# Performance work log

Measured on AMD Instinct MI355X. Metric: run time of the kernel, lower is better.

Reference implementation:

```python
import jax, jax.numpy as jnp
import numpy as np

B, V, C, H, W, D, G = 1, 5, 32, 128, 160, 48, 1


def _bilinear_sample(fea, x, y):
    # fea: [B,C,H,W]; x,y: [B,N] pixel coords (grid_sample align_corners=True, zero padding)
    Bb, Cc, Hh, Ww = fea.shape
    x0 = jnp.floor(x); y0 = jnp.floor(y)
    x1 = x0 + 1.0; y1 = y0 + 1.0
    wx1 = x - x0; wx0 = 1.0 - wx1
    wy1 = y - y0; wy0 = 1.0 - wy1
    flat = fea.reshape(Bb, Cc, Hh * Ww)
    def gather(xi, yi):
        valid = (xi >= 0) & (xi <= Ww - 1) & (yi >= 0) & (yi <= Hh - 1)
        xc = jnp.clip(xi, 0, Ww - 1).astype(jnp.int32)
        yc = jnp.clip(yi, 0, Hh - 1).astype(jnp.int32)
        idx = (yc * Ww + xc)[:, None, :]                      # [B,1,N]
        g = jnp.take_along_axis(flat, idx, axis=2)            # [B,C,N]
        return g * valid[:, None, :].astype(fea.dtype)
    return (gather(x0, y0) * (wx0 * wy0)[:, None, :]
          + gather(x1, y0) * (wx1 * wy0)[:, None, :]
          + gather(x0, y1) * (wx0 * wy1)[:, None, :]
          + gather(x1, y1) * (wx1 * wy1)[:, None, :])          # [B,C,N]


def _homo_warp(src_fea, src_proj, ref_proj, depth_values):
    # src_fea [B,C,H,W]; src_proj/ref_proj [B,4,4]; depth_values [B,D,H,W]
    Bb, Cc, Hh, Ww = src_fea.shape
    Dd = depth_values.shape[1]
    proj = src_proj @ jnp.linalg.inv(ref_proj)
    rot, trans = proj[:, :3, :3], proj[:, :3, 3:4]
    yy, xx = jnp.meshgrid(jnp.arange(Hh, dtype=src_fea.dtype),
                          jnp.arange(Ww, dtype=src_fea.dtype), indexing='ij')
    xyz = jnp.stack([xx.ravel(), yy.ravel(), jnp.ones(Hh * Ww, src_fea.dtype)], 0)  # [3,HW]
    rot_xyz = jnp.einsum('bij,jn->bin', rot, xyz)                                    # [B,3,HW]
    d = depth_values.reshape(Bb, 1, Dd, Hh * Ww)
    pxyz = rot_xyz[:, :, None, :] * d + trans[:, :, :, None]                         # [B,3,D,HW]
    px = (pxyz[:, 0] / pxyz[:, 2]).reshape(Bb, -1)
    py = (pxyz[:, 1] / pxyz[:, 2]).reshape(Bb, -1)
    warped = _bilinear_sample(src_fea, px, py)                                       # [B,C,D*HW]
    return warped.reshape(Bb, Cc, Dd, Hh, Ww)


def _pixelwise_net(sim, w0, b0, w1, b1, w2, b2):
    # sim [B,G,D,H,W]; 1x1x1 convs; BatchNorm at default init in eval is identity
    x = jax.nn.relu(jnp.einsum('oc,bcdhw->bodhw', w0, sim) + b0[None, :, None, None, None])
    x = jax.nn.relu(jnp.einsum('oc,bcdhw->bodhw', w1, x) + b1[None, :, None, None, None])
    x = jnp.einsum('oc,bcdhw->bodhw', w2, x) + b2[None, :, None, None, None]
    p = jax.nn.sigmoid(x[:, 0])                       # [B,D,H,W]
    return jnp.max(p, axis=1, keepdims=True)          # [B,1,H,W]


def _fuse_proj(p):
    # p [B,2,4,4] -> extrinsics with K folded into top 3x4
    top = jnp.einsum('bij,bjk->bik', p[:, 1, :3, :3], p[:, 0, :3, :4])
    return p[:, 0].at[:, :3, :4].set(top)


def _forward(features, proj_matrices, depth_values, w0, b0, w1, b1, w2, b2, reg_w, reg_b, num_depth):
    ref_fea = features[0]
    Bb, Cc, Hh, Ww = ref_fea.shape
    ref_proj = _fuse_proj(proj_matrices[:, 0])
    ref_vol = ref_fea.reshape(Bb, G, Cc // G, 1, Hh, Ww)
    sim_sum = 0.0
    wsum = 1e-5
    vw_list = []
    for i in range(1, features.shape[0]):
        src_proj = _fuse_proj(proj_matrices[:, i])
        warped = _homo_warp(features[i], src_proj, ref_proj, depth_values)
        warped = warped.reshape(Bb, G, Cc // G, num_depth, Hh, Ww)
        sim = (warped * ref_vol).mean(2)              # [B,G,D,H,W]
        vw = _pixelwise_net(sim, w0, b0, w1, b1, w2, b2)   # [B,1,H,W]
        vw_list.append(vw)
        sim_sum = sim_sum + sim * vw[:, None]
        wsum = wsum + vw[:, None]
    sim = sim_sum / wsum
    cost = jax.lax.conv_general_dilated(sim, reg_w, (1, 1, 1), 'SAME',
                                        dimension_numbers=('NCDHW', 'OIDHW', 'NCDHW'))
    prob_volume_pre = cost[:, 0] + reg_b[0]           # [B,D,H,W]
    prob = jax.nn.softmax(prob_volume_pre, axis=1)
    idx = jnp.argmax(prob, axis=1, keepdims=True)
    depth = jnp.take_along_axis(depth_values, idx, axis=1)[:, 0]   # winner-take-all depth
    conf = jnp.max(prob, axis=1)
    view_weights = jnp.concatenate(vw_list, axis=1)
    return depth, conf, prob, view_weights


def setup_inputs() -> dict:
    key = jax.random.key(0)
    ks = jax.random.split(key, 6)
    features = jax.random.normal(ks[0], (V, B, C, H, W), jnp.float32)
    # Plausible camera geometry: identity-ish extrinsics + pinhole intrinsics
    K = np.eye(4, dtype=np.float32)
    K[0, 0] = K[1, 1] = 150.0; K[0, 2] = W / 2.0; K[1, 2] = H / 2.0
    mats = []
    for v in range(V):
        E = np.eye(4, dtype=np.float32)
        a = 0.01 * v
        ca, sa = np.cos(a), np.sin(a)
        E[:3, :3] = np.array([[ca, 0, sa], [0, 1, 0], [-sa, 0, ca]], np.float32)
        E[0, 3] = -5.0 * v
        mats.append(np.stack([E, K], 0))
    proj_matrices = jnp.asarray(np.stack(mats, 0)[None])  # [1,V,2,4,4]
    depth_values = jnp.broadcast_to(
        jnp.linspace(425.0, 935.0, D, dtype=jnp.float32).reshape(1, D, 1, 1), (B, D, H, W)) * jnp.ones((B, D, H, W), jnp.float32)
    return {
        'features': features,
        'proj_matrices': proj_matrices,
        'depth_values': depth_values,
        'w0': jax.random.normal(ks[1], (16, G), jnp.float32) * 0.1,
        'b0': jnp.zeros((16,), jnp.float32),
        'w1': jax.random.normal(ks[2], (8, 16), jnp.float32) * 0.1,
        'b1': jnp.zeros((8,), jnp.float32),
        'w2': jax.random.normal(ks[3], (1, 8), jnp.float32) * 0.1,
        'b2': jnp.zeros((1,), jnp.float32),
        'reg_w': jax.random.normal(ks[4], (1, G, 3, 3, 3), jnp.float32) * 0.1,
        'reg_b': jnp.zeros((1,), jnp.float32),
        'num_depth': D,
    }


def reference(features, proj_matrices, depth_values, w0, b0, w1, b1, w2, b2, reg_w, reg_b, num_depth):
    return _forward(features, proj_matrices, depth_values, w0, b0, w1, b1, w2, b2, reg_w, reg_b, num_depth)
```

## Files before the change

kernel.cpp:

```cpp
#include <hip/hip_runtime.h>
#include <hip/hip_bf16.h>
#include <math.h>

#define W_  160
#define H_  128
#define HW  20480
#define D_  48
#define C_  32
#define NV  4

#define TX  16
#define TY  4
#define TXH 18
#define TYH 6
#define NCOL (TXH*TYH)

template<int CTRL>
__device__ __forceinline__ float dpp_add(float s) {
  int t = __builtin_amdgcn_update_dpp(0, __float_as_int(s), CTRL, 0xF, 0xF, true);
  return s + __int_as_float(t);
}

__device__ __forceinline__ unsigned ordf(float f) {
  unsigned b = __float_as_uint(f);
  return b ^ (((int)b >> 31) | 0x80000000u);
}
__device__ __forceinline__ float deordf(unsigned u) {
  unsigned b = (u & 0x80000000u) ? (u ^ 0x80000000u) : ~u;
  return __uint_as_float(b);
}

__device__ __forceinline__ void fuse_proj(const float* pm, float* P) {
  const float* E = pm;
  const float* K = pm + 16;
  for (int r = 0; r < 3; ++r)
    for (int c = 0; c < 4; ++c)
      P[r*4+c] = K[r*4+0]*E[0*4+c] + K[r*4+1]*E[1*4+c] + K[r*4+2]*E[2*4+c];
  for (int c = 0; c < 4; ++c) P[12+c] = E[12+c];
}

__device__ void invert4(const float* m, float* invOut) {
  float inv[16];
  inv[0]  =  m[5]*m[10]*m[15] - m[5]*m[11]*m[14] - m[9]*m[6]*m[15] + m[9]*m[7]*m[14] + m[13]*m[6]*m[11] - m[13]*m[7]*m[10];
  inv[4]  = -m[4]*m[10]*m[15] + m[4]*m[11]*m[14] + m[8]*m[6]*m[15] - m[8]*m[7]*m[14] - m[12]*m[6]*m[11] + m[12]*m[7]*m[10];
  inv[8]  =  m[4]*m[9]*m[15]  - m[4]*m[11]*m[13] - m[8]*m[5]*m[15] + m[8]*m[7]*m[13] + m[12]*m[5]*m[11] - m[12]*m[7]*m[9];
  inv[12] = -m[4]*m[9]*m[14]  + m[4]*m[10]*m[13] + m[8]*m[5]*m[14] - m[8]*m[6]*m[13] - m[12]*m[5]*m[10] + m[12]*m[6]*m[9];
  inv[1]  = -m[1]*m[10]*m[15] + m[1]*m[11]*m[14] + m[9]*m[2]*m[15] - m[9]*m[3]*m[14] - m[13]*m[2]*m[11] + m[13]*m[3]*m[10];
  inv[5]  =  m[0]*m[10]*m[15] - m[0]*m[11]*m[14] - m[8]*m[2]*m[15] + m[8]*m[3]*m[14] + m[12]*m[2]*m[11] - m[12]*m[3]*m[10];
  inv[9]  = -m[0]*m[9]*m[15]  + m[0]*m[11]*m[13] + m[8]*m[1]*m[15] - m[8]*m[3]*m[13] - m[12]*m[1]*m[11] + m[12]*m[3]*m[9];
  inv[13] =  m[0]*m[9]*m[14]  - m[0]*m[10]*m[13] - m[8]*m[1]*m[14] + m[8]*m[2]*m[13] + m[12]*m[1]*m[10] - m[12]*m[2]*m[9];
  inv[2]  =  m[1]*m[6]*m[15]  - m[1]*m[7]*m[14]  - m[5]*m[2]*m[15] + m[5]*m[3]*m[14] + m[13]*m[2]*m[7]  - m[13]*m[3]*m[6];
  inv[6]  = -m[0]*m[6]*m[15]  + m[0]*m[7]*m[14]  + m[4]*m[2]*m[15] - m[4]*m[3]*m[14] - m[12]*m[2]*m[7]  + m[12]*m[3]*m[6];
  inv[10] =  m[0]*m[5]*m[15]  - m[0]*m[7]*m[13]  - m[4]*m[1]*m[15] + m[4]*m[3]*m[13] + m[12]*m[1]*m[7]  - m[12]*m[3]*m[5];
  inv[14] = -m[0]*m[5]*m[14]  + m[0]*m[6]*m[13]  + m[4]*m[1]*m[14] - m[4]*m[2]*m[13] - m[12]*m[1]*m[6]  + m[12]*m[2]*m[5];
  inv[3]  = -m[1]*m[6]*m[11]  + m[1]*m[7]*m[10]  + m[5]*m[2]*m[11] - m[5]*m[3]*m[10] - m[9]*m[2]*m[7]   + m[9]*m[3]*m[6];
  inv[7]  =  m[0]*m[6]*m[11]  - m[0]*m[7]*m[10]  - m[4]*m[2]*m[11] + m[4]*m[3]*m[10] + m[8]*m[2]*m[7]   - m[8]*m[3]*m[6];
  inv[11] = -m[0]*m[5]*m[11]  + m[0]*m[7]*m[9]   + m[4]*m[1]*m[11] - m[4]*m[3]*m[9]  - m[8]*m[1]*m[7]   + m[8]*m[3]*m[5];
  inv[15] =  m[0]*m[5]*m[10]  - m[0]*m[6]*m[9]   - m[4]*m[1]*m[10] + m[4]*m[2]*m[9]  + m[8]*m[1]*m[6]   - m[8]*m[2]*m[5];
  float det = m[0]*inv[0] + m[1]*inv[4] + m[2]*inv[8] + m[3]*inv[12];
  det = 1.0f / det;
  for (int i = 0; i < 16; i++) invOut[i] = inv[i] * det;
}

__global__ void __launch_bounds__(256)
k_prep(const float* __restrict__ feat, const float* __restrict__ pm,
       float* __restrict__ tf, float* __restrict__ xf,
       unsigned* __restrict__ vwu) {
  __shared__ float tile[C_][64+1];
  int v  = blockIdx.y;
  int p0 = blockIdx.x * 64;
  int t  = threadIdx.x;

  if (v == 0) vwu[blockIdx.x*256 + t] = 0u;

  int pl = t & 63;
  int cg = t >> 6;
  const float* src = feat + (size_t)v*C_*HW + p0 + pl;
  #pragma unroll
  for (int k = 0; k < 8; ++k) {
    int c = cg*8 + k;
    tile[c][pl] = src[(size_t)c*HW];
  }
  __syncthreads();

  int pp = t >> 2;
  int co = (t & 3) * 8;
  float4 a, b;
  a.x = tile[co+0][pp]; a.y = tile[co+1][pp]; a.z = tile[co+2][pp]; a.w = tile[co+3][pp];
  b.x = tile[co+4][pp]; b.y = tile[co+5][pp]; b.z = tile[co+6][pp]; b.w = tile[co+7][pp];
  float* dst = tf + ((size_t)v*HW + p0 + pp)*C_ + co;
  *(float4*)dst = a;
  *(float4*)(dst+4) = b;

  if (blockIdx.x == 0 && v == 0) {
    if (t < 64) tf[(size_t)5*HW*C_ + t] = 0.0f;
    if (t == 0) {
      float Pr[16], Pinv[16], Ps[16], M[16];
      fuse_proj(pm, Pr);
      invert4(Pr, Pinv);
      for (int vv = 1; vv <= NV; ++vv) {
        fuse_proj(pm + vv*32, Ps);
        for (int r = 0; r < 4; ++r)
          for (int c = 0; c < 4; ++c) {
            float acc = 0.f;
            for (int k = 0; k < 4; ++k) acc += Ps[r*4+k]*Pinv[k*4+c];
            M[r*4+c] = acc;
          }
        float* o = xf + (vv-1)*12;
        o[0]=M[0];  o[1]=M[1];  o[2]=M[2];
        o[3]=M[4];  o[4]=M[5];  o[5]=M[6];
        o[6]=M[8];  o[7]=M[9];  o[8]=M[10];
        o[9]=M[3];  o[10]=M[7]; o[11]=M[11];
      }
    }
  }
}

template<int KX>
__device__ __forceinline__ void build_tab(
    const char* tfb, int chb, int ZB, float4 rfc,
    int xmin, int ymin, int ch, float* tabp ) {
  #pragma unroll
  for (int t = 0; t < KX*3; ++t) {
    int xi = xmin + t/3;
    int yi = ymin + t%3;
    bool valid = ((unsigned)xi < (unsigned)W_) && ((unsigned)yi < (unsigned)H_);
    int off = valid ? (yi*W_ + xi)*(C_*4) : ZB;
    float4 a = *(const float4*)(tfb + off + chb);
    float d = a.x*rfc.x + a.y*rfc.y + a.z*rfc.z + a.w*rfc.w;
    d = dpp_add<0xB1>(d);
    d = dpp_add<0x4E>(d);
    d = dpp_add<0x141>(d);
    if (ch == (t & 7)) tabp[t] = d;
  }
}

__global__ void __launch_bounds__(256)
k_warp(const float* __restrict__ tf, const float* __restrict__ dv,
       const float* __restrict__ xf, float* __restrict__ sim_all) {
  __shared__ float dtab[4][8][25];

  int lane = threadIdx.x & 63;
  int wv = threadIdx.x >> 6;
  int ch = lane & 7;
  int pix = (lane >> 3) & 7;
  int wvg = __builtin_amdgcn_readfirstlane((blockIdx.x*256 + threadIdx.x) >> 6);
  const int PGPV = HW/8;
  int pg = wvg % PGPV;
  int v  = wvg / PGPV;
  int p  = pg*8 + pix;

  float xpix = (float)(p % W_);
  float ypix = (float)(p / W_);

  const float* M = xf + v*12;
  float rx = M[0]*xpix + M[1]*ypix + M[2];
  float ry = M[3]*xpix + M[4]*ypix + M[5];
  float rz = M[6]*xpix + M[7]*ypix + M[8];
  float t0 = M[9], t1 = M[10], t2 = M[11];

  float4 rfc = *(const float4*)(tf + (size_t)p*C_ + ch*4);
  rfc.x *= (1.0f/(float)C_); rfc.y *= (1.0f/(float)C_);
  rfc.z *= (1.0f/(float)C_); rfc.w *= (1.0f/(float)C_);

  const char* tfb = (const char*)(tf + (size_t)(v+1)*HW*C_);
  const int chb = ch*16;
  const int ZB = (4-v)*HW*C_*4;

  float depE0 = dv[p];
  float depE1 = dv[(size_t)47*HW + p];
  float dpk[6];
  #pragma unroll
  for (int k = 0; k < 6; ++k) dpk[k] = dv[(size_t)(k*8 + ch)*HW + p];

  float Z0 = rz*depE0 + t2, Z1 = rz*depE1 + t2;
  float iz0 = 1.0f / Z0,     iz1 = 1.0f / Z1;
  float pxa = (rx*depE0 + t0) * iz0, pya = (ry*depE0 + t1) * iz0;
  float pxb = (rx*depE1 + t0) * iz1, pyb = (ry*depE1 + t1) * iz1;
  int xmin = (int)floorf(fminf(pxa, pxb));
  int ymin = (int)floorf(fminf(pya, pyb));
  int Nx = (int)floorf(fmaxf(pxa, pxb)) - xmin + 2;
  int Ny = (int)floorf(fmaxf(pya, pyb)) - ymin + 2;

  float dmn = fminf(depE0, depE1), dmx = fmaxf(depE0, depE1);
  bool ok = (Nx <= 8) && (Ny <= 3) && (Z0*Z1 > 0.0f);
  #pragma unroll
  for (int k = 0; k < 6; ++k) ok = ok && (dpk[k] >= dmn) && (dpk[k] <= dmx);

  float* simv = sim_all + (size_t)v*D_*HW + p;

  if (__all(ok)) {
    float* tabp = dtab[wv][pix];
    if (__all(Nx <= 5)) build_tab<5>(tfb, chb, ZB, rfc, xmin, ymin, ch, tabp);
    else                build_tab<8>(tfb, chb, ZB, rfc, xmin, ymin, ch, tabp);

    int xhi = xmin + 6;
    if (__all(Nx <= 5)) xhi = xmin + 3;

    #pragma unroll
    for (int k = 0; k < 6; ++k) {
      float dep = dpk[k];
      float Z  = rz*dep + t2;
      float zr = 1.0f / Z;
      float px = (rx*dep + t0) * zr;
      float py = (ry*dep + t1) * zr;
      int xi = (int)floorf(px);
      int yi = (int)floorf(py);
      xi = min(max(xi, xmin), xhi);
      yi = min(max(yi, ymin), ymin + 1);
      float wx1 = px - (float)xi;
      float wy1 = py - (float)yi;
      float wx0 = 1.0f - wx1, wy0 = 1.0f - wy1;
      int idx = (xi - xmin)*3 + (yi - ymin);
      float t00 = tabp[idx];
      float t01 = tabp[idx + 3];
      float t10 = tabp[idx + 1];
      float t11 = tabp[idx + 4];
      float s = wx0*wy0*t00 + wx1*wy0*t01 + wx0*wy1*t10 + wx1*wy1*t11;
      simv[(size_t)(k*8 + ch)*HW] = s;
    }
  } else {
    const float* tff  = tf + (size_t)(v+1)*HW*C_;
    const float* refp = tf + (size_t)p*C_;
    const int ZE = (4-v)*HW*C_;
    #pragma unroll 1
    for (int k = 0; k < 6; ++k) {
      float dep = dpk[k];
      float Z  = rz*dep + t2;
      float px = (rx*dep + t0) / Z;
      float py = (ry*dep + t1) / Z;
      float x0f = floorf(px), y0f = floorf(py);
      float wx1 = px - x0f, wy1 = py - y0f;
      float wx0 = 1.0f - wx1, wy0 = 1.0f - wy1;
      int x0 = (int)x0f, y0 = (int)y0f;
      int x1 = x0 + 1,   y1 = y0 + 1;
      bool vx0 = ((unsigned)x0 <= (unsigned)(W_-1));
      bool vx1 = ((unsigned)x1 <= (unsigned)(W_-1));
      bool vy0 = ((unsigned)y0 <= (unsigned)(H_-1));
      bool vy1 = ((unsigned)y1 <= (unsigned)(H_-1));
      int cx0 = min(max(x0, 0), W_-1);
      int cx1 = min(max(x1, 0), W_-1);
      int cy0 = min(max(y0, 0), H_-1);
      int cy1 = min(max(y1, 0), H_-1);
      int o00 = (vx0 && vy0) ? (cy0*W_+cx0)*C_ : ZE;
      int o01 = (vx1 && vy0) ? (cy0*W_+cx1)*C_ : ZE;
      int o10 = (vx0 && vy1) ? (cy1*W_+cx0)*C_ : ZE;
      int o11 = (vx1 && vy1) ? (cy1*W_+cx1)*C_ : ZE;
      float a00=0.f, a01=0.f, a10=0.f, a11=0.f;
      #pragma unroll 1
      for (int q = 0; q < 8; ++q) {
        float4 rq = *(const float4*)(refp + q*4);
        float4 c0 = *(const float4*)(tff + o00 + q*4);
        float4 c1 = *(const float4*)(tff + o01 + q*4);
        float4 c2 = *(const float4*)(tff + o10 + q*4);
        float4 c3 = *(const float4*)(tff + o11 + q*4);
        a00 += c0.x*rq.x + c0.y*rq.y + c0.z*rq.z + c0.w*rq.w;
        a01 += c1.x*rq.x + c1.y*rq.y + c1.z*rq.z + c1.w*rq.w;
        a10 += c2.x*rq.x + c2.y*rq.y + c2.z*rq.z + c2.w*rq.w;
        a11 += c3.x*rq.x + c3.y*rq.y + c3.z*rq.z + c3.w*rq.w;
      }
      float s = (wx0*wy0*a00 + wx1*wy0*a01 + wx0*wy1*a10 + wx1*wy1*a11)
                * (1.0f/(float)C_);
      simv[(size_t)(k*8 + ch)*HW] = s;
    }
  }
}

__global__ void __launch_bounds__(256)
k_mlp(const float* __restrict__ sim_all,
      const float* __restrict__ w0, const float* __restrict__ b0,
      const float* __restrict__ w1, const float* __restrict__ b1,
      const float* __restrict__ w2, const float* __restrict__ b2,
      unsigned* __restrict__ vwu) {
  int idx = blockIdx.x*blockDim.x + threadIdx.x;
  if (idx >= NV*(D_/4)*HW) return;
  int p = idx % HW;
  int t = idx / HW;
  int v = t / (D_/4);
  int c = t % (D_/4);

  const float* sp_ = sim_all + ((size_t)(v*D_ + c*4))*HW + p;
  float sv[4];
  sv[0] = sp_[0];
  sv[1] = sp_[HW];
  sv[2] = sp_[2*HW];
  sv[3] = sp_[3*HW];

  float ymax = -3.0e38f;
  #pragma unroll
  for (int k = 0; k < 4; ++k) {
    float s = sv[k];
    float acc0 = b1[0], acc1 = b1[1], acc2 = b1[2], acc3 = b1[3];
    float acc4 = b1[4], acc5 = b1[5], acc6 = b1[6], acc7 = b1[7];
    #pragma unroll
    for (int o = 0; o < 16; ++o) {
      float h = fmaxf(fmaf(w0[o], s, b0[o]), 0.0f);
      acc0 = fmaf(w1[0*16+o], h, acc0);
      acc1 = fmaf(w1[1*16+o], h, acc1);
      acc2 = fmaf(w1[2*16+o], h, acc2);
      acc3 = fmaf(w1[3*16+o], h, acc3);
      acc4 = fmaf(w1[4*16+o], h, acc4);
      acc5 = fmaf(w1[5*16+o], h, acc5);
      acc6 = fmaf(w1[6*16+o], h, acc6);
      acc7 = fmaf(w1[7*16+o], h, acc7);
    }
    float yv = b2[0];
    yv = fmaf(w2[0], fmaxf(acc0, 0.0f), yv);
    yv = fmaf(w2[1], fmaxf(acc1, 0.0f), yv);
    yv = fmaf(w2[2], fmaxf(acc2, 0.0f), yv);
    yv = fmaf(w2[3], fmaxf(acc3, 0.0f), yv);
    yv = fmaf(w2[4], fmaxf(acc4, 0.0f), yv);
    yv = fmaf(w2[5], fmaxf(acc5, 0.0f), yv);
    yv = fmaf(w2[6], fmaxf(acc6, 0.0f), yv);
    yv = fmaf(w2[7], fmaxf(acc7, 0.0f), yv);
    ymax = fmaxf(ymax, yv);
  }
  atomicMax(&vwu[(size_t)v*HW + p], ordf(ymax));
}

__global__ void __launch_bounds__(256)
k_fct(const float* __restrict__ sim_all, const unsigned* __restrict__ vwu,
      const float* __restrict__ rw, const float* __restrict__ rb,
      const float* __restrict__ dv, float* __restrict__ out) {
  __shared__ float sfus[D_][TYH][TXH+1];
  __shared__ float scost[D_][64];
  __shared__ float svw[NV][NCOL];
  __shared__ float sinvw[NCOL];
  __shared__ int   sgpc[NCOL];

  int tid = threadIdx.x;
  int gx0 = blockIdx.x*TX;
  int gy0 = blockIdx.y*TY;

  if (tid < NCOL) {
    int yy = tid / TXH, xx = tid % TXH;
    int gy = gy0 + yy - 1, gx = gx0 + xx - 1;
    bool valid = (gx >= 0) && (gx < W_) && (gy >= 0) && (gy < H_);
    int gp = min(max(gy,0),H_-1)*W_ + min(max(gx,0),W_-1);
    sgpc[tid] = gp;
    float a0 = 1.0f/(1.0f + expf(-deordf(vwu[0*HW+gp])));
    float a1 = 1.0f/(1.0f + expf(-deordf(vwu[1*HW+gp])));
    float a2 = 1.0f/(1.0f + expf(-deordf(vwu[2*HW+gp])));
    float a3 = 1.0f/(1.0f + expf(-deordf(vwu[3*HW+gp])));
    float inv = valid ? 1.0f/(1e-5f + a0+a1+a2+a3) : 0.0f;
    if (!valid) { a0=a1=a2=a3=0.f; }
    svw[0][tid]=a0; svw[1][tid]=a1; svw[2][tid]=a2; svw[3][tid]=a3;
    sinvw[tid] = inv;
  }
  __syncthreads();

  for (int j = tid; j < D_*NCOL; j += 256) {
    int d = j / NCOL, r = j % NCOL;
    int gp = sgpc[r];
    float s0 = sim_all[(size_t)(0*D_+d)*HW + gp];
    float s1 = sim_all[(size_t)(1*D_+d)*HW + gp];
    float s2 = sim_all[(size_t)(2*D_+d)*HW + gp];
    float s3 = sim_all[(size_t)(3*D_+d)*HW + gp];
    float val = (s0*svw[0][r] + s1*svw[1][r] + s2*svw[2][r] + s3*svw[3][r]) * sinvw[r];
    int yy = r / TXH, xx = r % TXH;
    sfus[d][yy][xx] = val;
  }
  __syncthreads();

  {
    int pid = tid & 63;
    int dg  = tid >> 6;
    int px = pid & 15, py = pid >> 4;
    float kw[27];
    #pragma unroll
    for (int i = 0; i < 27; ++i) kw[i] = rw[i];
    float bias = rb[0];

    float pm1[9], p0[9], pp1[9];
    int d0 = dg*12;
    #pragma unroll
    for (int i = 0; i < 9; ++i) {
      int ky = i/3, kx = i%3;
      pm1[i] = (d0 > 0) ? sfus[d0-1][py+ky][px+kx] : 0.0f;
      p0[i]  = sfus[d0][py+ky][px+kx];
    }
    #pragma unroll
    for (int k = 0; k < 12; ++k) {
      int d = d0 + k;
      #pragma unroll
      for (int i = 0; i < 9; ++i) {
        int ky = i/3, kx = i%3;
        pp1[i] = (d+1 < D_) ? sfus[d+1][py+ky][px+kx] : 0.0f;
      }
      float acc = bias;
      #pragma unroll
      for (int i = 0; i < 9; ++i) acc += pm1[i]*kw[i];
      #pragma unroll
      for (int i = 0; i < 9; ++i) acc += p0[i]*kw[9+i];
      #pragma unroll
      for (int i = 0; i < 9; ++i) acc += pp1[i]*kw[18+i];
      scost[d][pid] = acc;
      #pragma unroll
      for (int i = 0; i < 9; ++i) { pm1[i] = p0[i]; p0[i] = pp1[i]; }
    }
  }
  __syncthreads();

  if (tid < 64) {
    int tx = tid & 15, ty = tid >> 4;
    int gx = gx0 + tx, gy = gy0 + ty;
    int gp = gy*W_ + gx;
    float vmax = scost[0][tid];
    int am = 0;
    #pragma unroll
    for (int d = 1; d < D_; ++d) {
      float c = scost[d][tid];
      if (c > vmax) { vmax = c; am = d; }
    }
    float sum = 0.0f;
    #pragma unroll
    for (int d = 0; d < D_; ++d) {
      float e = expf(scost[d][tid] - vmax);
      scost[d][tid] = e;
      sum += e;
    }
    float inv = 1.0f / sum;
    #pragma unroll
    for (int d = 0; d < D_; ++d)
      out[(size_t)(2*HW) + (size_t)d*HW + gp] = scost[d][tid] * inv;
    out[gp] = dv[(size_t)am*HW + gp];
    out[HW + gp] = inv;
    int rint = (ty+1)*TXH + (tx+1);
    #pragma unroll
    for (int v = 0; v < NV; ++v)
      out[(size_t)(2*HW + D_*HW) + (size_t)v*HW + gp] = svw[v][rint];
  }
}

extern "C" void kernel_launch(void* const* d_in, const int* in_sizes, int n_in,
                              void* d_out, int out_size, void* d_ws, size_t ws_size,
                              hipStream_t stream) {
  const float* feat = (const float*)d_in[0];
  const float* pm   = (const float*)d_in[1];
  const float* dv   = (const float*)d_in[2];
  const float* w0   = (const float*)d_in[3];
  const float* b0   = (const float*)d_in[4];
  const float* w1   = (const float*)d_in[5];
  const float* b1   = (const float*)d_in[6];
  const float* w2   = (const float*)d_in[7];
  const float* b2   = (const float*)d_in[8];
  const float* rw   = (const float*)d_in[9];
  const float* rb   = (const float*)d_in[10];
  float* out = (float*)d_out;
  float* ws  = (float*)d_ws;

  float*    xf  = ws;
  float*    tf  = ws + 64;
  float*    sim = ws + 3276928;
  unsigned* vwu = (unsigned*)(ws + 7209088);

  hipLaunchKernelGGL(k_prep, dim3(HW/64, 5), dim3(256), 0, stream,
                     feat, pm, tf, xf, vwu);
  hipLaunchKernelGGL(k_warp, dim3((NV*HW*8)/256), dim3(256), 0, stream,
                     tf, dv, xf, sim);
  hipLaunchKernelGGL(k_mlp, dim3((NV*(D_/4)*HW)/256), dim3(256), 0, stream,
                     sim, w0, b0, w1, b1, w2, b2, vwu);
  hipLaunchKernelGGL(k_fct, dim3(W_/TX, H_/TY), dim3(256), 0, stream,
                     sim, vwu, rw, rb, dv, out);
}
```

Measured before the change: 74.79 us.

## Split fused cost-volume kernel into depth-chunked 3D conv and per-pixel softmax kernels

Replaces the single k_fct kernel, which handled all 48 depths per tile, with two kernels. k_fusecv splits depth into 4 groups across blockIdx.z so the grid is four times larger, and writes the conv output to a global cost buffer. k_softmax then reads that buffer per pixel to do argmax, softmax and the view-weight outputs. This raises parallelism and lowers shared memory per block, at the price of an extra launch, a global round trip for the cost volume, and recomputing halo depth slices.

```diff
diff --git a/kernel.cpp b/kernel.cpp
--- a/kernel.cpp
+++ b/kernel.cpp
@@ -14,6 +14,8 @@
 #define TXH 18
 #define TYH 6
 #define NCOL (TXH*TYH)
+#define GD  4
+#define GDS 12
 
 template<int CTRL>
 __device__ __forceinline__ float dpp_add(float s) {
@@ -119,7 +121,7 @@
 template<int KX>
 __device__ __forceinline__ void build_tab(
     const char* tfb, int chb, int ZB, float4 rfc,
-    int xmin, int ymin, int ch, float* tabp ) {
+    int xmin, int ymin, int ch, float* tabp) {
   #pragma unroll
   for (int t = 0; t < KX*3; ++t) {
     int xi = xmin + t/3;
@@ -319,18 +321,18 @@
 }
 
 __global__ void __launch_bounds__(256)
-k_fct(const float* __restrict__ sim_all, const unsigned* __restrict__ vwu,
-      const float* __restrict__ rw, const float* __restrict__ rb,
-      const float* __restrict__ dv, float* __restrict__ out) {
-  __shared__ float sfus[D_][TYH][TXH+1];
-  __shared__ float scost[D_][64];
+k_fusecv(const float* __restrict__ sim_all, const unsigned* __restrict__ vwu,
+         const float* __restrict__ rw, const float* __restrict__ rb,
+         float* __restrict__ cost) {
   __shared__ float svw[NV][NCOL];
   __shared__ float sinvw[NCOL];
   __shared__ int   sgpc[NCOL];
+  __shared__ float sfus[GDS+2][TYH][TXH+1];
 
   int tid = threadIdx.x;
   int gx0 = blockIdx.x*TX;
   int gy0 = blockIdx.y*TY;
+  int g   = blockIdx.z;
 
   if (tid < NCOL) {
     int yy = tid / TXH, xx = tid % TXH;
@@ -349,16 +351,19 @@
   }
   __syncthreads();
 
-  for (int j = tid; j < D_*NCOL; j += 256) {
-    int d = j / NCOL, r = j % NCOL;
-    int gp = sgpc[r];
-    float s0 = sim_all[(size_t)(0*D_+d)*HW + gp];
-    float s1 = sim_all[(size_t)(1*D_+d)*HW + gp];
-    float s2 = sim_all[(size_t)(2*D_+d)*HW + gp];
-    float s3 = sim_all[(size_t)(3*D_+d)*HW + gp];
-    float val = (s0*svw[0][r] + s1*svw[1][r] + s2*svw[2][r] + s3*svw[3][r]) * sinvw[r];
-    int yy = r / TXH, xx = r % TXH;
-    sfus[d][yy][xx] = val;
+  for (int j = tid; j < (GDS+2)*NCOL; j += 256) {
+    int s = j / NCOL, r = j % NCOL;
+    int dz = g*GDS - 1 + s;
+    float val = 0.0f;
+    if (dz >= 0 && dz < D_) {
+      int gp = sgpc[r];
+      float s0 = sim_all[(size_t)(0*D_+dz)*HW + gp];
+      float s1 = sim_all[(size_t)(1*D_+dz)*HW + gp];
+      float s2 = sim_all[(size_t)(2*D_+dz)*HW + gp];
+      float s3 = sim_all[(size_t)(3*D_+dz)*HW + gp];
+      val = (s0*svw[0][r] + s1*svw[1][r] + s2*svw[2][r] + s3*svw[3][r]) * sinvw[r];
+    }
+    sfus[s][r/TXH][r%TXH] = val;
   }
   __syncthreads();
 
@@ -370,66 +375,58 @@
     #pragma unroll
     for (int i = 0; i < 27; ++i) kw[i] = rw[i];
     float bias = rb[0];
-
-    float pm1[9], p0[9], pp1[9];
-    int d0 = dg*12;
+    int gp = (gy0+py)*W_ + gx0+px;
+
     #pragma unroll
-    for (int i = 0; i < 9; ++i) {
-      int ky = i/3, kx = i%3;
-      pm1[i] = (d0 > 0) ? sfus[d0-1][py+ky][px+kx] : 0.0f;
-      p0[i]  = sfus[d0][py+ky][px+kx];
-    }
-    #pragma unroll
-    for (int k = 0; k < 12; ++k) {
-      int d = d0 + k;
-      #pragma unroll
-      for (int i = 0; i < 9; ++i) {
-        int ky = i/3, kx = i%3;
-        pp1[i] = (d+1 < D_) ? sfus[d+1][py+ky][px+kx] : 0.0f;
-      }
+    for (int k = 0; k < 3; ++k) {
+      int dl = dg*3 + k;
       float acc = bias;
       #pragma unroll
-      for (int i = 0; i < 9; ++i) acc += pm1[i]*kw[i];
-      #pragma unroll
-      for (int i = 0; i < 9; ++i) acc += p0[i]*kw[9+i];
-      #pragma unroll
-      for (int i = 0; i < 9; ++i) acc += pp1[i]*kw[18+i];
-      scost[d][pid] = acc;
-      #pragma unroll
-      for (int i = 0; i < 9; ++i) { pm1[i] = p0[i]; p0[i] = pp1[i]; }
-    }
-  }
-  __syncthreads();
-
-  if (tid < 64) {
-    int tx = tid & 15, ty = tid >> 4;
-    int gx = gx0 + tx, gy = gy0 + ty;
-    int gp = gy*W_ + gx;
-    float vmax = scost[0][tid];
-    int am = 0;
-    #pragma unroll
-    for (int d = 1; d < D_; ++d) {
-      float c = scost[d][tid];
-      if (c > vmax) { vmax = c; am = d; }
-    }
-    float sum = 0.0f;
-    #pragma unroll
-    for (int d = 0; d < D_; ++d) {
-      float e = expf(scost[d][tid] - vmax);
-      scost[d][tid] = e;
-      sum += e;
-    }
-    float inv = 1.0f / sum;
-    #pragma unroll
-    for (int d = 0; d < D_; ++d)
-      out[(size_t)(2*HW) + (size_t)d*HW + gp] = scost[d][tid] * inv;
-    out[gp] = dv[(size_t)am*HW + gp];
-    out[HW + gp] = inv;
-    int rint = (ty+1)*TXH + (tx+1);
-    #pragma unroll
-    for (int v = 0; v < NV; ++v)
-      out[(size_t)(2*HW + D_*HW) + (size_t)v*HW + gp] = svw[v][rint];
-  }
+      for (int kd = 0; kd < 3; ++kd)
+        #pragma unroll
+        for (int ky = 0; ky < 3; ++ky)
+          #pragma unroll
+          for (int kx = 0; kx < 3; ++kx)
+            acc += sfus[dl+kd][py+ky][px+kx] * kw[(kd*3+ky)*3+kx];
+      cost[(size_t)(g*GDS + dl)*HW + gp] = acc;
+    }
+  }
+}
+
+__global__ void __launch_bounds__(256)
+k_softmax(const float* __restrict__ cost, const unsigned* __restrict__ vwu,
+          const float* __restrict__ dv, float* __restrict__ out) {
+  int p = blockIdx.x*256 + threadIdx.x;
+  if (p >= HW) return;
+
+  float c[D_];
+  #pragma unroll
+  for (int d = 0; d < D_; ++d) c[d] = cost[(size_t)d*HW + p];
+
+  float vmax = c[0];
+  int am = 0;
+  #pragma unroll
+  for (int d = 1; d < D_; ++d) {
+    if (c[d] > vmax) { vmax = c[d]; am = d; }
+  }
+  float sum = 0.0f;
+  #pragma unroll
+  for (int d = 0; d < D_; ++d) {
+    float e = expf(c[d] - vmax);
+    c[d] = e;
+    sum += e;
+  }
+  float inv = 1.0f / sum;
+  #pragma unroll
+  for (int d = 0; d < D_; ++d)
+    out[(size_t)(2*HW) + (size_t)d*HW + p] = c[d] * inv;
+
+  out[p] = dv[(size_t)am*HW + p];
+  out[HW + p] = inv;
+  #pragma unroll
+  for (int v = 0; v < NV; ++v)
+    out[(size_t)(2*HW + D_*HW) + (size_t)v*HW + p] =
+        1.0f/(1.0f + expf(-deordf(vwu[(size_t)v*HW + p])));
 }
 
 extern "C" void kernel_launch(void* const* d_in, const int* in_sizes, int n_in,
@@ -449,10 +446,11 @@
   float* out = (float*)d_out;
   float* ws  = (float*)d_ws;
 
-  float*    xf  = ws;
-  float*    tf  = ws + 64;
-  float*    sim = ws + 3276928;
-  unsigned* vwu = (unsigned*)(ws + 7209088);
+  float*    xf   = ws;
+  float*    tf   = ws + 64;
+  float*    sim  = ws + 3276928;
+  unsigned* vwu  = (unsigned*)(ws + 7209088);
+  float*    cost = ws + 7291008;
 
   hipLaunchKernelGGL(k_prep, dim3(HW/64, 5), dim3(256), 0, stream,
                      feat, pm, tf, xf, vwu);
@@ -460,6 +458,8 @@
                      tf, dv, xf, sim);
   hipLaunchKernelGGL(k_mlp, dim3((NV*(D_/4)*HW)/256), dim3(256), 0, stream,
                      sim, w0, b0, w1, b1, w2, b2, vwu);
-  hipLaunchKernelGGL(k_fct, dim3(W_/TX, H_/TY), dim3(256), 0, stream,
-                     sim, vwu, rw, rb, dv, out);
-}
+  hipLaunchKernelGGL(k_fusecv, dim3(W_/TX, H_/TY, GD), dim3(256), 0, stream,
+                     sim, vwu, rw, rb, cost);
+  hipLaunchKernelGGL(k_softmax, dim3(HW/256), dim3(256), 0, stream,
+                     cost, vwu, dv, out);
+}
```

Measured after the change: 75.38 us. About the same (+0.8%).
